# Optimization experiments

Hardware: AMD Instinct MI355X
Metric: run time of the kernel (lower is better)

The kernel has to match this reference:

```python
import jax, jax.numpy as jnp
import numpy as np


def _gcn(x, src, dst, W, b, n):
    # GCNConv: x' = D^{-1/2} (A + I) D^{-1/2} (x W) + b  (self-loops added)
    loop = jnp.arange(n, dtype=src.dtype)
    s = jnp.concatenate([src, loop])
    d = jnp.concatenate([dst, loop])
    deg = jax.ops.segment_sum(jnp.ones(s.shape[0], x.dtype), d, num_segments=n)
    dis = jnp.where(deg > 0, jax.lax.rsqrt(deg), jnp.zeros_like(deg))
    h = x @ W  # [n, out]
    msg = h[s] * (dis[s] * dis[d])[:, None]  # [E+n, out]
    return jax.ops.segment_sum(msg, d, num_segments=n) + b


def setup_inputs() -> dict:
    key = jax.random.key(0)
    ks = jax.random.split(key, 12)
    N0, N1, N2, N3, N4 = 100000, 200000, 400000, 800000, 1600000
    DEG = 6  # avg mesh degree

    def glorot(k, fi, fo):
        return jax.random.normal(k, (fi, fo), jnp.float32) * np.float32(np.sqrt(2.0 / (fi + fo)))

    def ei(k, n):
        return jax.random.randint(k, (2, DEG * n), 0, n, dtype=jnp.int32)

    return {
        "x": jax.random.normal(ks[0], (N0, 3), jnp.float32),
        "W1": glorot(ks[1], 3, 32), "b1": jnp.zeros((32,), jnp.float32),
        "W2": glorot(ks[2], 32, 64), "b2": jnp.zeros((64,), jnp.float32),
        "W3": glorot(ks[3], 64, 32), "b3": jnp.zeros((32,), jnp.float32),
        "W4": glorot(ks[4], 32, 3), "b4": jnp.zeros((3,), jnp.float32),
        "edge_index0": ei(ks[5], N0),
        "unpool1": jax.random.randint(ks[6], (N1,), 0, N0, dtype=jnp.int32),
        "edge_index1": ei(ks[7], N1),
        "unpool2": jax.random.randint(ks[8], (N2,), 0, N1, dtype=jnp.int32),
        "edge_index2": ei(ks[9], N2),
        "unpool3": jax.random.randint(ks[10], (N3,), 0, N2, dtype=jnp.int32),
        "edge_index3": ei(ks[11], N3),
        "unpool4": jax.random.randint(jax.random.fold_in(key, 99), (N4,), 0, N3, dtype=jnp.int32),
    }


def reference(x, W1, b1, W2, b2, W3, b3, W4, b4,
              edge_index0, unpool1, edge_index1, unpool2,
              edge_index2, unpool3, edge_index3, unpool4):
    N0 = x.shape[0]
    N1, N2, N3 = unpool1.shape[0], unpool2.shape[0], unpool3.shape[0]
    h = jax.nn.relu(_gcn(x, edge_index0[0], edge_index0[1], W1, b1, N0))
    h = h[unpool1]  # mesh_unpool stage 1: gather to finer mesh
    h = jax.nn.relu(_gcn(h, edge_index1[0], edge_index1[1], W2, b2, N1))
    h = h[unpool2]
    h = jax.nn.relu(_gcn(h, edge_index2[0], edge_index2[1], W3, b3, N2))
    h = h[unpool3]
    h = jax.nn.relu(_gcn(h, edge_index3[0], edge_index3[1], W4, b4, N3))
    return h[unpool4]  # final unpooled vertex features [N4, 3]
```

## Files before the change

kernel.cpp:

```cpp
#include <hip/hip_runtime.h>
#include <hip/hip_bf16.h>

typedef __hip_bfloat16 bf16;
typedef unsigned short u16;
typedef unsigned char u8;
typedef unsigned int u32;
typedef __attribute__((ext_vector_type(8))) unsigned short us8;

static __device__ __forceinline__ float b2f(bf16 v) { return __bfloat162float(v); }
static __device__ __forceinline__ float bfu2f(u32 u) {
    union { u32 i; float f; } c; c.i = u << 16; return c.f;
}
static __device__ __forceinline__ u16 f2bfu(float f) {
    u32 x = __float_as_uint(f);
    return (u16)((x + 0x7FFFu + ((x >> 16) & 1u)) >> 16);
}

#define TILE 4096
#define CBITS 12
#define CRANGE 4096
#define OUTB 26624
#define WF_W1 0
#define WF_B1 128
#define WF_W2 192
#define WF_B2 2240
#define WF_W3 2304
#define WF_W4 4352
#define WF_TOT 4608
#define RPT16(M) M(0) M(1) M(2) M(3) M(4) M(5) M(6) M(7) \
                 M(8) M(9) M(10) M(11) M(12) M(13) M(14) M(15)

struct SP {
    const int* src; const int* dst;
    int E, N, cap, nb, nblk, nbpad;
    int* gcur;
    u32* pairs;
    int* M;
    int* rowptr; float* dis; int* csr;
};
struct Pack {
    SP s[4];
    int poff[4];
    int boff[4];
};

__global__ void k_detect(const u16* __restrict__ xraw, int* __restrict__ flag) {
    __shared__ int s;
    if (threadIdx.x == 0) s = 0;
    __syncthreads();
    u16 u = xraw[threadIdx.x];
    int e = (u >> 7) & 0xFF;
    if (e >= 0x8F) atomicAdd(&s, 1);
    __syncthreads();
    if (threadIdx.x == 0) flag[0] = (s > 0) ? 1 : 0;
}

__global__ void k_prep_w(const void* W1, const void* b1, const void* W2,
                         const void* b2, const void* W3, const void* W4,
                         float* __restrict__ wf, const int* __restrict__ flag) {
    int t = blockIdx.x * 256 + threadIdx.x;
    int f32m = flag[0];
    const void* src; int off; int len;
    if      (t < WF_B1)  { src = W1; off = t - WF_W1; len = 96;  }
    else if (t < WF_W2)  { src = b1; off = t - WF_B1; len = 32;  }
    else if (t < WF_B2)  { src = W2; off = t - WF_W2; len = 2048;}
    else if (t < WF_W3)  { src = b2; off = t - WF_B2; len = 64;  }
    else if (t < WF_W4)  { src = W3; off = t - WF_W3; len = 2048;}
    else if (t < WF_TOT) { src = W4; off = t - WF_W4; len = 96;  }
    else return;
    if (off >= len) return;
    wf[t] = f32m ? ((const float*)src)[off] : b2f(((const bf16*)src)[off]);
}

__global__ void k_init(int* __restrict__ gcur_all, Pack pk) {
    int i = blockIdx.x * blockDim.x + threadIdx.x;
    if (i < 1024) gcur_all[i] = 0;
    if (i < 4) pk.s[i].rowptr[pk.s[i].N] = pk.s[i].E;
}

__global__ void __launch_bounds__(256) k_part_hist(Pack pk) {
    __shared__ int hist[256];
    int bid = blockIdx.x;
    int si = (bid >= pk.poff[3]) ? 3 : (bid >= pk.poff[2]) ? 2 : (bid >= pk.poff[1]) ? 1 : 0;
    const SP sp = pk.s[si];
    int lb = bid - pk.poff[si];
    int t = threadIdx.x;
    int n = min(TILE, sp.E - lb * TILE);
    const int* dstp = sp.dst + lb * TILE;

#define LOADK(k) int d##k; { int i = t + 256*(k); d##k = (i < n) ? dstp[i] : -1; }
    RPT16(LOADK)
#undef LOADK
    hist[t] = 0;
    __syncthreads();
#define HISTK(k) if (d##k >= 0) atomicAdd(&hist[d##k >> CBITS], 1);
    RPT16(HISTK)
#undef HISTK
    __syncthreads();
    int* Mrow = sp.M + (size_t)lb * sp.nbpad;
    for (int b = t; b < sp.nb; b += 256) Mrow[b] = hist[b];
}

__global__ void __launch_bounds__(256) k_part_scan(Pack pk) {
    __shared__ int buf[256];
    int bid = blockIdx.x;
    int si = (bid >= pk.boff[3]) ? 3 : (bid >= pk.boff[2]) ? 2 : (bid >= pk.boff[1]) ? 1 : 0;
    const SP sp = pk.s[si];
    int b = bid - pk.boff[si];
    int t = threadIdx.x;
    int nblk = sp.nblk, nbpad = sp.nbpad;
    int* M = sp.M;
    int carry = 0;
    for (int base = 0; base < nblk; base += 256) {
        int m = min(256, nblk - base);
        int v = (t < m) ? M[(size_t)(base + t) * nbpad + b] : 0;
        buf[t] = v;
        __syncthreads();
        for (int off = 1; off < 256; off <<= 1) {
            int w = (t >= off) ? buf[t - off] : 0;
            __syncthreads();
            buf[t] += w;
            __syncthreads();
        }
        int excl = buf[t] - v + carry;
        int ctot = buf[255];
        __syncthreads();
        if (t < m) M[(size_t)(base + t) * nbpad + b] = excl;
        carry += ctot;
    }
    if (t == 0) sp.gcur[b] = carry;
}

__global__ void __launch_bounds__(256) k_partition(Pack pk) {
    __shared__ u32 stage[TILE];
    __shared__ u8  bkt[TILE];
    __shared__ int hist[256];
    __shared__ int gofs[256];
    __shared__ int tmp[256];

    int bid = blockIdx.x;
    int si = (bid >= pk.poff[3]) ? 3 : (bid >= pk.poff[2]) ? 2 : (bid >= pk.poff[1]) ? 1 : 0;
    const SP sp = pk.s[si];
    int lb = bid - pk.poff[si];
    int t = threadIdx.x;
    int n = min(TILE, sp.E - lb * TILE);
    const int* dstp = sp.dst + lb * TILE;
    const int* srcp = sp.src + lb * TILE;

#define LOADK(k) int d##k, s##k; { int i = t + 256*(k); \
    if (i < n) { d##k = dstp[i]; s##k = srcp[i]; } else { d##k = -1; s##k = 0; } }
    RPT16(LOADK)
#undef LOADK

    hist[t] = 0;
    __syncthreads();
#define HISTK(k) if (d##k >= 0) atomicAdd(&hist[d##k >> CBITS], 1);
    RPT16(HISTK)
#undef HISTK
    __syncthreads();

    int h = hist[t];
    tmp[t] = h; __syncthreads();
    for (int off = 1; off < 256; off <<= 1) {
        int v = (t >= off) ? tmp[t - off] : 0;
        __syncthreads();
        tmp[t] += v;
        __syncthreads();
    }
    int lofs = tmp[t] - h;
    int gb = (t < sp.nb) ? sp.M[(size_t)lb * sp.nbpad + t] : 0;
    gofs[t] = gb - lofs;
    hist[t] = lofs;
    __syncthreads();

#define SCATK(k) if (d##k >= 0) { int b = d##k >> CBITS; \
    int pos = atomicAdd(&hist[b], 1); \
    stage[pos] = (((u32)d##k & 4095u) << 20) | (u32)s##k; \
    bkt[pos] = (u8)b; }
    RPT16(SCATK)
#undef SCATK
    __syncthreads();

    int cap = sp.cap;
    u32* pairs = sp.pairs;
    for (int i = t; i < n; i += 256) {
        int b = bkt[i];
        pairs[(size_t)b * cap + gofs[b] + i] = stage[i];
    }
}

__global__ void k_scan_bbase(Pack pk, int* __restrict__ bbase_all) {
    __shared__ int tmp[256];
    int si = blockIdx.x;
    int t = threadIdx.x;
    int nb = pk.s[si].nb;
    int v = (t < nb) ? pk.s[si].gcur[t] : 0;
    tmp[t] = v; __syncthreads();
    for (int off = 1; off < 256; off <<= 1) {
        int w = (t >= off) ? tmp[t - off] : 0;
        __syncthreads();
        tmp[t] += w;
        __syncthreads();
    }
    bbase_all[si * 256 + t] = tmp[t] - v;
}

__global__ void __launch_bounds__(512) k_build(Pack pk, const int* __restrict__ bbase_all) {
    __shared__ int hist[4096];
    __shared__ int outb[OUTB];
    __shared__ int tmp[512];

    int bid = blockIdx.x;
    int si = (bid >= pk.boff[3]) ? 3 : (bid >= pk.boff[2]) ? 2 : (bid >= pk.boff[1]) ? 1 : 0;
    const SP sp = pk.s[si];
    int b = bid - pk.boff[si];
    int t = threadIdx.x;

    int bbase = bbase_all[si * 256 + b];
    int tot = sp.gcur[b];
    const u32* p = sp.pairs + (size_t)b * sp.cap;
    const uint4* p4 = (const uint4*)p;
    int tot4 = tot >> 2;

    for (int i = t; i < 4096; i += 512) hist[i] = 0;
    __syncthreads();
    for (int i = t; i < tot4; i += 512) {
        uint4 u = p4[i];
        atomicAdd(&hist[u.x >> 20], 1);
        atomicAdd(&hist[u.y >> 20], 1);
        atomicAdd(&hist[u.z >> 20], 1);
        atomicAdd(&hist[u.w >> 20], 1);
    }
    for (int i = (tot4 << 2) + t; i < tot; i += 512)
        atomicAdd(&hist[p[i] >> 20], 1);
    __syncthreads();

    int lbase = t * 8;
    int cnt[8], cof[8];
    #pragma unroll
    for (int k = 0; k < 8; k++) cnt[k] = hist[lbase + k];
    int s = 0;
    #pragma unroll
    for (int k = 0; k < 8; k++) { cof[k] = s; s += cnt[k]; }
    tmp[t] = s; __syncthreads();
    for (int off = 1; off < 512; off <<= 1) {
        int v = (t >= off) ? tmp[t - off] : 0;
        __syncthreads();
        tmp[t] += v;
        __syncthreads();
    }
    int tb = tmp[t] - s;

    int nbase = b << CBITS;
    #pragma unroll
    for (int k = 0; k < 8; k++) {
        int bin = lbase + k;
        hist[bin] = tb + cof[k];
        int v = nbase + bin;
        if (v < sp.N) {
            sp.rowptr[v] = bbase + tb + cof[k];
            sp.dis[v] = rsqrtf((float)(cnt[k] + 1));
        }
    }
    __syncthreads();

    if (tot <= OUTB) {
        for (int i = t; i < tot4; i += 512) {
            uint4 u = p4[i];
            int pos;
            pos = atomicAdd(&hist[u.x >> 20], 1); outb[pos] = (int)(u.x & 0xFFFFFu);
            pos = atomicAdd(&hist[u.y >> 20], 1); outb[pos] = (int)(u.y & 0xFFFFFu);
            pos = atomicAdd(&hist[u.z >> 20], 1); outb[pos] = (int)(u.z & 0xFFFFFu);
            pos = atomicAdd(&hist[u.w >> 20], 1); outb[pos] = (int)(u.w & 0xFFFFFu);
        }
        for (int i = (tot4 << 2) + t; i < tot; i += 512) {
            u32 u = p[i];
            int pos = atomicAdd(&hist[u >> 20], 1);
            outb[pos] = (int)(u & 0xFFFFFu);
        }
        __syncthreads();
        for (int i = t; i < tot; i += 512)
            sp.csr[bbase + i] = outb[i];
    } else {
        for (int i = t; i < tot; i += 512) {
            u32 u = p[i];
            int pos = atomicAdd(&hist[u >> 20], 1);
            sp.csr[bbase + pos] = (int)(u & 0xFFFFFu);
        }
    }
}

template <int F, bool EXT>
__global__ void k_pre(const void* __restrict__ xin, const int* __restrict__ gidx,
                      const bf16* __restrict__ actin, const float* __restrict__ dis,
                      bf16* __restrict__ g, const int* __restrict__ flag, int total) {
    int i = blockIdx.x * blockDim.x + threadIdx.x;
    if (i >= total) return;
    int v = i / F;
    int f = i - v * F;
    float x;
    if (EXT) {
        if (flag[0]) x = ((const float*)xin)[i];
        else         x = b2f(((const bf16*)xin)[i]);
    } else {
        int row = gidx[v];
        x = b2f(actin[(size_t)row * F + f]);
    }
    g[i] = __float2bfloat16(dis[v] * x);
}

__global__ void __launch_bounds__(256, 1) k_fuse_mm_pre(
        const bf16* __restrict__ xt1, const int* __restrict__ up,
        const float* __restrict__ wf, const float* __restrict__ dis,
        bf16* __restrict__ g, int n) {
    const float* W = wf + WF_W1;
    const float* B = wf + WF_B1;
    int v = blockIdx.x * 256 + threadIdx.x;
    if (v >= n) return;
    int r = up[v];
    float x0 = b2f(xt1[(size_t)r * 3 + 0]);
    float x1 = b2f(xt1[(size_t)r * 3 + 1]);
    float x2 = b2f(xt1[(size_t)r * 3 + 2]);
    float dv = dis[v];
    #pragma unroll
    for (int f8 = 0; f8 < 4; f8++) {
        us8 ov;
        #pragma unroll
        for (int j = 0; j < 8; j++) {
            int f = f8 * 8 + j;
            float y = B[f];
            y = fmaf(x0, W[f], y);
            y = fmaf(x1, W[32 + f], y);
            y = fmaf(x2, W[64 + f], y);
            y = y > 0.f ? y : 0.f;
            ov[j] = f2bfu(dv * y);
        }
        *(us8*)(g + (size_t)v * 32 + f8 * 8) = ov;
    }
}

__global__ void __launch_bounds__(256, 1) k_fuse_mm2(
        const bf16* __restrict__ xt2, const float* __restrict__ wf,
        bf16* __restrict__ h, int n) {
    __shared__ float Xs[256 * 33];
    const float* W2f = wf + WF_W2;
    const float* B2f = wf + WF_B2;
    const float* W3f = wf + WF_W3;
    int v = blockIdx.x * 256 + threadIdx.x;
    if (v >= n) return;
    float* xs = &Xs[threadIdx.x * 33];
    #pragma unroll
    for (int k8 = 0; k8 < 4; k8++) {
        us8 xv = *(const us8*)(xt2 + (size_t)v * 32 + k8 * 8);
        #pragma unroll
        for (int j = 0; j < 8; j++) xs[k8 * 8 + j] = bfu2f((u32)(u16)xv[j]);
    }
    float acc[32];
    #pragma unroll
    for (int f = 0; f < 32; f++) acc[f] = 0.f;
    #pragma unroll
    for (int c = 0; c < 64; c += 32) {
        float y[32];
        #pragma unroll
        for (int f = 0; f < 32; f++) y[f] = B2f[c + f];
        #pragma unroll
        for (int k = 0; k < 32; k++) {
            float xk = xs[k];
            const float* wr = &W2f[k * 64 + c];
            #pragma unroll
            for (int f = 0; f < 32; f++) y[f] = fmaf(xk, wr[f], y[f]);
        }
        #pragma unroll
        for (int j = 0; j < 32; j++) {
            float yj = y[j] > 0.f ? y[j] : 0.f;
            const float* wr3 = &W3f[(c + j) * 32];
            #pragma unroll
            for (int f = 0; f < 32; f++) acc[f] = fmaf(yj, wr3[f], acc[f]);
        }
    }
    #pragma unroll
    for (int f8 = 0; f8 < 4; f8++) {
        us8 ov;
        #pragma unroll
        for (int j = 0; j < 8; j++) ov[j] = f2bfu(acc[f8 * 8 + j]);
        *(us8*)(h + (size_t)v * 32 + f8 * 8) = ov;
    }
}

template <int FIN, int FOUT>
__global__ void __launch_bounds__(256, 1) k_matmul_seq(
        const bf16* __restrict__ actin, const float* __restrict__ W,
        bf16* __restrict__ h, int n) {
    int v = blockIdx.x * blockDim.x + threadIdx.x;
    if (v >= n) return;
    float y[FOUT];
    #pragma unroll
    for (int f = 0; f < FOUT; f++) y[f] = 0.f;
    #pragma unroll
    for (int k8 = 0; k8 < FIN / 8; k8++) {
        us8 xv = *(const us8*)(actin + (size_t)v * FIN + k8 * 8);
        #pragma unroll
        for (int j = 0; j < 8; j++) {
            float xk = bfu2f((u32)(u16)xv[j]);
            const float* wrow = &W[(k8 * 8 + j) * FOUT];
            #pragma unroll
            for (int f = 0; f < FOUT; f++) y[f] = fmaf(xk, wrow[f], y[f]);
        }
    }
    if constexpr (FOUT % 8 == 0) {
        #pragma unroll
        for (int f8 = 0; f8 < FOUT / 8; f8++) {
            us8 ov;
            #pragma unroll
            for (int j = 0; j < 8; j++) ov[j] = f2bfu(y[f8 * 8 + j]);
            *(us8*)(h + (size_t)v * FOUT + f8 * 8) = ov;
        }
    } else {
        #pragma unroll
        for (int f = 0; f < FOUT; f++)
            h[(size_t)v * FOUT + f] = __float2bfloat16(y[f]);
    }
}

template <int FOUT, bool FINALIZE>
__global__ void __launch_bounds__(256) k_gather2v(
        const bf16* __restrict__ g, const int* __restrict__ rowptr,
        const int* __restrict__ csr, const float* __restrict__ dis,
        const void* __restrict__ bias, bf16* __restrict__ out,
        const int* __restrict__ flag, int totq, int E) {
    constexpr int Q = FOUT / 4;
    constexpr u32 W2 = FOUT / 2;
    int H = (totq + 1) >> 1;
    int i = blockIdx.x * blockDim.x + threadIdx.x;
    if (i >= H) return;
    int Em1 = E - 1;
    int e1 = i;
    int e2 = i + H;
    int e2c = (e2 < totq) ? e2 : e1;
    int v1 = e1 / Q, q1 = e1 - v1 * Q;
    int v2 = e2c / Q, q2 = e2c - v2 * Q;
    u32 qo1 = (u32)(q1 * 2), qo2 = (u32)(q2 * 2);
    const u32* g32 = (const u32*)g;

    uint2 sv1 = *(const uint2*)(g32 + (u32)v1 * W2 + qo1);
    uint2 sv2 = *(const uint2*)(g32 + (u32)v2 * W2 + qo2);
    float s10 = bfu2f(sv1.x & 0xFFFFu), s11 = bfu2f(sv1.x >> 16);
    float s12 = bfu2f(sv1.y & 0xFFFFu), s13 = bfu2f(sv1.y >> 16);
    float s20 = bfu2f(sv2.x & 0xFFFFu), s21 = bfu2f(sv2.x >> 16);
    float s22 = bfu2f(sv2.y & 0xFFFFu), s23 = bfu2f(sv2.y >> 16);

    int r1 = rowptr[v1]; int c1 = rowptr[v1 + 1] - r1;
    int r2 = rowptr[v2]; int c2 = rowptr[v2 + 1] - r2;
    int last1 = min(r1 + (c1 > 0 ? c1 - 1 : 0), Em1);
    int last2 = min(r2 + (c2 > 0 ? c2 - 1 : 0), Em1);
    int j1 = 0, j2 = 0;
    while (j1 < c1 || j2 < c2) {
        int i10 = min(r1 + j1 + 0, last1), i11 = min(r1 + j1 + 1, last1);
        int i12 = min(r1 + j1 + 2, last1), i13 = min(r1 + j1 + 3, last1);
        int i20 = min(r2 + j2 + 0, last2), i21 = min(r2 + j2 + 1, last2);
        int i22 = min(r2 + j2 + 2, last2), i23 = min(r2 + j2 + 3, last2);
        u32 u10 = (u32)csr[i10], u11 = (u32)csr[i11];
        u32 u12 = (u32)csr[i12], u13 = (u32)csr[i13];
        u32 u20 = (u32)csr[i20], u21 = (u32)csr[i21];
        u32 u22 = (u32)csr[i22], u23 = (u32)csr[i23];
        uint2 a10 = *(const uint2*)(g32 + u10 * W2 + qo1);
        uint2 a11 = *(const uint2*)(g32 + u11 * W2 + qo1);
        uint2 a12 = *(const uint2*)(g32 + u12 * W2 + qo1);
        uint2 a13 = *(const uint2*)(g32 + u13 * W2 + qo1);
        uint2 a20 = *(const uint2*)(g32 + u20 * W2 + qo2);
        uint2 a21 = *(const uint2*)(g32 + u21 * W2 + qo2);
        uint2 a22 = *(const uint2*)(g32 + u22 * W2 + qo2);
        uint2 a23 = *(const uint2*)(g32 + u23 * W2 + qo2);
        if (j1 + 0 >= c1) { a10.x = 0; a10.y = 0; }
        if (j1 + 1 >= c1) { a11.x = 0; a11.y = 0; }
        if (j1 + 2 >= c1) { a12.x = 0; a12.y = 0; }
        if (j1 + 3 >= c1) { a13.x = 0; a13.y = 0; }
        if (j2 + 0 >= c2) { a20.x = 0; a20.y = 0; }
        if (j2 + 1 >= c2) { a21.x = 0; a21.y = 0; }
        if (j2 + 2 >= c2) { a22.x = 0; a22.y = 0; }
        if (j2 + 3 >= c2) { a23.x = 0; a23.y = 0; }
        s10 += bfu2f(a10.x & 0xFFFFu) + bfu2f(a11.x & 0xFFFFu)
             + bfu2f(a12.x & 0xFFFFu) + bfu2f(a13.x & 0xFFFFu);
        s11 += bfu2f(a10.x >> 16) + bfu2f(a11.x >> 16)
             + bfu2f(a12.x >> 16) + bfu2f(a13.x >> 16);
        s12 += bfu2f(a10.y & 0xFFFFu) + bfu2f(a11.y & 0xFFFFu)
             + bfu2f(a12.y & 0xFFFFu) + bfu2f(a13.y & 0xFFFFu);
        s13 += bfu2f(a10.y >> 16) + bfu2f(a11.y >> 16)
             + bfu2f(a12.y >> 16) + bfu2f(a13.y >> 16);
        s20 += bfu2f(a20.x & 0xFFFFu) + bfu2f(a21.x & 0xFFFFu)
             + bfu2f(a22.x & 0xFFFFu) + bfu2f(a23.x & 0xFFFFu);
        s21 += bfu2f(a20.x >> 16) + bfu2f(a21.x >> 16)
             + bfu2f(a22.x >> 16) + bfu2f(a23.x >> 16);
        s22 += bfu2f(a20.y & 0xFFFFu) + bfu2f(a21.y & 0xFFFFu)
             + bfu2f(a22.y & 0xFFFFu) + bfu2f(a23.y & 0xFFFFu);
        s23 += bfu2f(a20.y >> 16) + bfu2f(a21.y >> 16)
             + bfu2f(a22.y >> 16) + bfu2f(a23.y >> 16);
        j1 += 4; j2 += 4;
    }
    float dv1 = dis[v1], dv2 = dis[v2];
    float o1[4] = {s10, s11, s12, s13};
    float o2[4] = {s20, s21, s22, s23};
    uint2 w1, w2;
    if (FINALIZE) {
        int f32m = flag[0];
        #pragma unroll
        for (int k = 0; k < 4; k++) {
            int f1 = q1 * 4 + k, f2 = q2 * 4 + k;
            float bf1 = f32m ? ((const float*)bias)[f1] : b2f(((const bf16*)bias)[f1]);
            float bf2 = f32m ? ((const float*)bias)[f2] : b2f(((const bf16*)bias)[f2]);
            o1[k] = fmaf(dv1, o1[k], bf1); o1[k] = o1[k] > 0.f ? o1[k] : 0.f;
            o2[k] = fmaf(dv2, o2[k], bf2); o2[k] = o2[k] > 0.f ? o2[k] : 0.f;
        }
    } else {
        #pragma unroll
        for (int k = 0; k < 4; k++) { o1[k] *= dv1; o2[k] *= dv2; }
    }
    w1.x = (u32)f2bfu(o1[0]) | ((u32)f2bfu(o1[1]) << 16);
    w1.y = (u32)f2bfu(o1[2]) | ((u32)f2bfu(o1[3]) << 16);
    w2.x = (u32)f2bfu(o2[0]) | ((u32)f2bfu(o2[1]) << 16);
    w2.y = (u32)f2bfu(o2[2]) | ((u32)f2bfu(o2[3]) << 16);
    u32* o32 = (u32*)out;
    *(uint2*)(o32 + (u32)v1 * W2 + qo1) = w1;
    if (e2 < totq) *(uint2*)(o32 + (u32)v2 * W2 + qo2) = w2;
}

template <int FOUT, bool FINALIZE>
__global__ void __launch_bounds__(256) k_gather2(
        const bf16* __restrict__ g, const int* __restrict__ rowptr,
        const int* __restrict__ csr, const float* __restrict__ dis,
        const void* __restrict__ bias, bf16* __restrict__ out,
        const int* __restrict__ flag, int total, int E) {
    int H = (total + 1) >> 1;
    int i = blockIdx.x * blockDim.x + threadIdx.x;
    if (i >= H) return;
    int Em1 = E - 1;
    int e1 = i;
    int e2 = i + H;
    int e2c = (e2 < total) ? e2 : e1;
    int v1 = e1 / FOUT, f1 = e1 - v1 * FOUT;
    int v2 = e2c / FOUT, f2 = e2c - v2 * FOUT;
    float s1 = b2f(g[e1]);
    float s2 = b2f(g[e2c]);
    int r1 = rowptr[v1]; int c1 = rowptr[v1 + 1] - r1;
    int r2 = rowptr[v2]; int c2 = rowptr[v2 + 1] - r2;
    int last1 = min(r1 + (c1 > 0 ? c1 - 1 : 0), Em1);
    int last2 = min(r2 + (c2 > 0 ? c2 - 1 : 0), Em1);
    int j1 = 0, j2 = 0;
    while (j1 < c1 || j2 < c2) {
        int i10 = min(r1 + j1 + 0, last1), i11 = min(r1 + j1 + 1, last1);
        int i12 = min(r1 + j1 + 2, last1), i13 = min(r1 + j1 + 3, last1);
        int i20 = min(r2 + j2 + 0, last2), i21 = min(r2 + j2 + 1, last2);
        int i22 = min(r2 + j2 + 2, last2), i23 = min(r2 + j2 + 3, last2);
        int u10 = csr[i10], u11 = csr[i11], u12 = csr[i12], u13 = csr[i13];
        int u20 = csr[i20], u21 = csr[i21], u22 = csr[i22], u23 = csr[i23];
        float a10 = b2f(g[(size_t)u10 * FOUT + f1]);
        float a11 = b2f(g[(size_t)u11 * FOUT + f1]);
        float a12 = b2f(g[(size_t)u12 * FOUT + f1]);
        float a13 = b2f(g[(size_t)u13 * FOUT + f1]);
        float a20 = b2f(g[(size_t)u20 * FOUT + f2]);
        float a21 = b2f(g[(size_t)u21 * FOUT + f2]);
        float a22 = b2f(g[(size_t)u22 * FOUT + f2]);
        float a23 = b2f(g[(size_t)u23 * FOUT + f2]);
        s1 += ((j1 + 0 < c1 ? a10 : 0.f) + (j1 + 1 < c1 ? a11 : 0.f))
            + ((j1 + 2 < c1 ? a12 : 0.f) + (j1 + 3 < c1 ? a13 : 0.f));
        s2 += ((j2 + 0 < c2 ? a20 : 0.f) + (j2 + 1 < c2 ? a21 : 0.f))
            + ((j2 + 2 < c2 ? a22 : 0.f) + (j2 + 3 < c2 ? a23 : 0.f));
        j1 += 4; j2 += 4;
    }
    float dv1 = dis[v1], dv2 = dis[v2];
    float o1, o2;
    if (FINALIZE) {
        float bf1 = flag[0] ? ((const float*)bias)[f1] : b2f(((const bf16*)bias)[f1]);
        float bf2 = flag[0] ? ((const float*)bias)[f2] : b2f(((const bf16*)bias)[f2]);
        o1 = fmaf(dv1, s1, bf1); o1 = o1 > 0.f ? o1 : 0.f;
        o2 = fmaf(dv2, s2, bf2); o2 = o2 > 0.f ? o2 : 0.f;
    } else {
        o1 = dv1 * s1;
        o2 = dv2 * s2;
    }
    out[e1] = __float2bfloat16(o1);
    if (e2 < total) out[e2] = __float2bfloat16(o2);
}

__global__ void k_gather_out(const bf16* __restrict__ act, const int* __restrict__ idx,
                             void* __restrict__ out, const int* __restrict__ flag, int n) {
    int u = blockIdx.x * blockDim.x + threadIdx.x;
    if (u >= n) return;
    size_t r = (size_t)idx[u];
    float v0 = b2f(act[3 * r + 0]);
    float v1 = b2f(act[3 * r + 1]);
    float v2 = b2f(act[3 * r + 2]);
    if (flag[0]) {
        float* o = (float*)out;
        o[3 * (size_t)u + 0] = v0; o[3 * (size_t)u + 1] = v1; o[3 * (size_t)u + 2] = v2;
    } else {
        bf16* o = (bf16*)out;
        o[3 * (size_t)u + 0] = __float2bfloat16(v0);
        o[3 * (size_t)u + 1] = __float2bfloat16(v1);
        o[3 * (size_t)u + 2] = __float2bfloat16(v2);
    }
}

static inline int cdiv(long long a, long long b) { return (int)((a + b - 1) / b); }

extern "C" void kernel_launch(void* const* d_in, const int* in_sizes, int n_in,
                              void* d_out, int out_size, void* d_ws, size_t ws_size,
                              hipStream_t stream) {
    const void* x  = d_in[0];
    const void* W1 = d_in[1]; const void* b1 = d_in[2];
    const void* W2 = d_in[3]; const void* b2 = d_in[4];
    const void* W3 = d_in[5]; const void* b3 = d_in[6];
    const void* W4 = d_in[7]; const void* b4 = d_in[8];
    const int* e0  = (const int*)d_in[9];
    const int* up1 = (const int*)d_in[10];
    const int* e1  = (const int*)d_in[11];
    const int* up2 = (const int*)d_in[12];
    const int* e2  = (const int*)d_in[13];
    const int* up3 = (const int*)d_in[14];
    const int* e3  = (const int*)d_in[15];
    const int* up4 = (const int*)d_in[16];

    const int N0 = in_sizes[0] / 3;
    const int N1 = in_sizes[10];
    const int N2 = in_sizes[12];
    const int N3 = in_sizes[14];
    const int N4 = in_sizes[16];
    const int E0 = in_sizes[9] / 2, E1 = in_sizes[11] / 2;
    const int E2 = in_sizes[13] / 2, E3 = in_sizes[15] / 2;

    int Ns[4] = {N0, N1, N2, N3};
    int Es[4] = {E0, E1, E2, E3};
    const int* srcs[4] = {e0, e1, e2, e3};
    const int* dsts[4] = {e0 + E0, e1 + E1, e2 + E2, e3 + E3};

    size_t gmax = (size_t)N0 * 3;
    if ((size_t)N1 * 32 > gmax) gmax = (size_t)N1 * 32;
    if ((size_t)N2 * 32 > gmax) gmax = (size_t)N2 * 32;
    if ((size_t)N3 * 3  > gmax) gmax = (size_t)N3 * 3;
    size_t amax = (size_t)N0 * 32;
    if ((size_t)N1 * 64 > amax) amax = (size_t)N1 * 64;
    if ((size_t)N2 * 32 > amax) amax = (size_t)N2 * 32;
    if ((size_t)N3 * 3  > amax) amax = (size_t)N3 * 3;
    gmax = (gmax + 7) & ~(size_t)7;
    amax = (amax + 7) & ~(size_t)7;

    Pack pk;
    char* p = (char*)d_ws;
    int* flag = (int*)p;            p += 256;
    float* wf = (float*)p;          p += WF_TOT * 4;
    int* gcur_all = (int*)p;        p += 1024 * 4;
    int* bbase_all = (int*)p;       p += 1024 * 4;

    for (int s = 0; s < 4; s++) {
        pk.s[s].src = srcs[s]; pk.s[s].dst = dsts[s];
        pk.s[s].E = Es[s]; pk.s[s].N = Ns[s];
        int nb = cdiv(Ns[s], CRANGE);
        pk.s[s].nb = nb;
        pk.s[s].nblk = cdiv(Es[s], TILE);
        pk.s[s].nbpad = (nb + 15) & ~15;
        pk.s[s].cap = (Es[s] / nb + Es[s] / (8 * nb) + 256 + 3) & ~3;
        pk.s[s].gcur = gcur_all + s * 256;
        pk.s[s].M = (int*)p;        p += (size_t)pk.s[s].nblk * pk.s[s].nbpad * 4;
        pk.s[s].rowptr = (int*)p;   p += ((size_t)(Ns[s] + 1 + 3) & ~(size_t)3) * 4;
        pk.s[s].dis = (float*)p;    p += ((size_t)(Ns[s] + 3) & ~(size_t)3) * 4;
    }
    for (int s = 0; s < 4; s++) {
        pk.s[s].csr = (int*)p;      p += ((size_t)(Es[s] + 3) & ~(size_t)3) * 4;
    }

    char* U = (char*)(((size_t)p + 15) & ~(size_t)15);
    size_t pairsBytes = 0;
    for (int s = 0; s < 4; s++) {
        pk.s[s].pairs = (u32*)(U + pairsBytes);
        pairsBytes += (size_t)pk.s[s].cap * pk.s[s].nb * 4;
    }
    bf16* g   = (bf16*)U;
    bf16* act = g + gmax;
    bf16* xt  = act + amax;

    int ptot = 0, btot = 0;
    for (int s = 0; s < 4; s++) {
        pk.poff[s] = ptot; ptot += pk.s[s].nblk;
        pk.boff[s] = btot; btot += pk.s[s].nb;
    }

    const int B = 256;

    k_detect<<<1, 256, 0, stream>>>((const u16*)x, flag);
    k_prep_w<<<cdiv(WF_TOT, B), B, 0, stream>>>(W1, b1, W2, b2, W3, W4, wf, flag);
    k_init<<<4, 256, 0, stream>>>(gcur_all, pk);
    k_part_hist<<<ptot, B, 0, stream>>>(pk);
    k_part_scan<<<btot, B, 0, stream>>>(pk);
    k_partition<<<ptot, B, 0, stream>>>(pk);
    k_scan_bbase<<<4, B, 0, stream>>>(pk, bbase_all);
    k_build<<<btot, 512, 0, stream>>>(pk, bbase_all);

    {
        int T = N0 * 3, Hh = (T + 1) >> 1;
        k_pre<3, true><<<cdiv(T, B), B, 0, stream>>>(
            x, nullptr, nullptr, pk.s[0].dis, g, flag, T);
        k_gather2<3, false><<<cdiv(Hh, B), B, 0, stream>>>(
            g, pk.s[0].rowptr, pk.s[0].csr, pk.s[0].dis, nullptr, xt, flag, T, E0);
    }

    k_fuse_mm_pre<<<cdiv(N1, B), B, 0, stream>>>(
        xt, up1, wf, pk.s[1].dis, g, N1);

    {
        int Tq = N1 * 8, Hq = (Tq + 1) >> 1;
        k_gather2v<32, false><<<cdiv(Hq, B), B, 0, stream>>>(
            g, pk.s[1].rowptr, pk.s[1].csr, pk.s[1].dis, nullptr, xt, flag, Tq, E1);
    }

    k_fuse_mm2<<<cdiv(N1, B), B, 0, stream>>>(xt, wf, act, N1);

    {
        int Tq = N2 * 8, Hq = (Tq + 1) >> 1;
        k_pre<32, false><<<cdiv((long long)N2 * 32, B), B, 0, stream>>>(
            nullptr, up2, act, pk.s[2].dis, g, flag, N2 * 32);
        k_gather2v<32, true><<<cdiv(Hq, B), B, 0, stream>>>(
            g, pk.s[2].rowptr, pk.s[2].csr, pk.s[2].dis, b3, act, flag, Tq, E2);
    }

    {
        int T = N3 * 3, Hh = (T + 1) >> 1;
        k_matmul_seq<32, 3><<<cdiv(N2, B), B, 0, stream>>>(act, wf + WF_W4, xt, N2);
        k_pre<3, false><<<cdiv(T, B), B, 0, stream>>>(
            nullptr, up3, xt, pk.s[3].dis, g, flag, T);
        k_gather2<3, true><<<cdiv(Hh, B), B, 0, stream>>>(
            g, pk.s[3].rowptr, pk.s[3].csr, pk.s[3].dis, b4, act, flag, T, E3);
    }

    k_gather_out<<<cdiv(N4, B), B, 0, stream>>>(act, up4, d_out, flag, N4);
}
```

Measured before the change: 465.0 us.

## Compute fused W2/W3 matmul with bf16 MFMA instead of scalar FMAs

Rewrites the fused 32->64->32 layer-2/layer-3 matmul to use 16x16x32 bf16 MFMA instructions, with each wavefront handling 16 rows. The weight-prep kernel now also builds pre-swizzled bf16 MFMA B-fragments of W2 and W3. The intermediate ReLU activations are rounded to bf16 and staged through shared memory, which adds a precision loss compared with the fp32 scalar path. The goal is to replace about 4K scalar FMAs per row, which ran at one block per CU with heavy register use.

```diff
diff --git a/kernel.cpp b/kernel.cpp
--- a/kernel.cpp
+++ b/kernel.cpp
@@ -6,6 +6,8 @@
 typedef unsigned char u8;
 typedef unsigned int u32;
 typedef __attribute__((ext_vector_type(8))) unsigned short us8;
+typedef __attribute__((ext_vector_type(8))) short short8;
+typedef __attribute__((ext_vector_type(4))) float f32x4;
 
 static __device__ __forceinline__ float b2f(bf16 v) { return __bfloat162float(v); }
 static __device__ __forceinline__ float bfu2f(u32 u) {
@@ -27,6 +29,7 @@
 #define WF_W3 2304
 #define WF_W4 4352
 #define WF_TOT 4608
+#define NFRAG 4096
 #define RPT16(M) M(0) M(1) M(2) M(3) M(4) M(5) M(6) M(7) \
                  M(8) M(9) M(10) M(11) M(12) M(13) M(14) M(15)
 
@@ -57,19 +60,39 @@
 
 __global__ void k_prep_w(const void* W1, const void* b1, const void* W2,
                          const void* b2, const void* W3, const void* W4,
-                         float* __restrict__ wf, const int* __restrict__ flag) {
+                         float* __restrict__ wf, u16* __restrict__ wfrag,
+                         const int* __restrict__ flag) {
     int t = blockIdx.x * 256 + threadIdx.x;
     int f32m = flag[0];
-    const void* src; int off; int len;
-    if      (t < WF_B1)  { src = W1; off = t - WF_W1; len = 96;  }
-    else if (t < WF_W2)  { src = b1; off = t - WF_B1; len = 32;  }
-    else if (t < WF_B2)  { src = W2; off = t - WF_W2; len = 2048;}
-    else if (t < WF_W3)  { src = b2; off = t - WF_B2; len = 64;  }
-    else if (t < WF_W4)  { src = W3; off = t - WF_W3; len = 2048;}
-    else if (t < WF_TOT) { src = W4; off = t - WF_W4; len = 96;  }
-    else return;
-    if (off >= len) return;
-    wf[t] = f32m ? ((const float*)src)[off] : b2f(((const bf16*)src)[off]);
+    if (t < WF_TOT) {
+        const void* src; int off; int len;
+        if      (t < WF_B1)  { src = W1; off = t - WF_W1; len = 96;  }
+        else if (t < WF_W2)  { src = b1; off = t - WF_B1; len = 32;  }
+        else if (t < WF_B2)  { src = W2; off = t - WF_W2; len = 2048;}
+        else if (t < WF_W3)  { src = b2; off = t - WF_B2; len = 64;  }
+        else if (t < WF_W4)  { src = W3; off = t - WF_W3; len = 2048;}
+        else                 { src = W4; off = t - WF_W4; len = 96;  }
+        if (off >= len) return;
+        wf[t] = f32m ? ((const float*)src)[off] : b2f(((const bf16*)src)[off]);
+    } else if (t < WF_TOT + NFRAG) {
+        int idx = t - WF_TOT;
+        int sec = idx >> 9;
+        int l = (idx >> 3) & 63;
+        int i = idx & 7;
+        int cl = l & 15, grp = l >> 4;
+        float val;
+        if (sec < 4) {
+            int k = grp * 8 + i, col = sec * 16 + cl;
+            val = f32m ? ((const float*)W2)[k * 64 + col]
+                       : b2f(((const bf16*)W2)[k * 64 + col]);
+        } else {
+            int q = sec - 4, kt = q >> 1, t2 = q & 1;
+            int k = kt * 32 + grp * 8 + i, col = t2 * 16 + cl;
+            val = f32m ? ((const float*)W3)[k * 32 + col]
+                       : b2f(((const bf16*)W3)[k * 32 + col]);
+        }
+        wfrag[idx] = f2bfu(val);
+    }
 }
 
 __global__ void k_init(int* __restrict__ gcur_all, Pack pk) {
@@ -339,52 +362,49 @@
     }
 }
 
-__global__ void __launch_bounds__(256, 1) k_fuse_mm2(
-        const bf16* __restrict__ xt2, const float* __restrict__ wf,
-        bf16* __restrict__ h, int n) {
-    __shared__ float Xs[256 * 33];
-    const float* W2f = wf + WF_W2;
+__global__ void __launch_bounds__(256) k_fuse_mm2(
+        const bf16* __restrict__ xt2, const u16* __restrict__ wfrag,
+        const float* __restrict__ wf, bf16* __restrict__ h, int n) {
+    __shared__ u16 Ys[4][16 * 72];
+    __shared__ u16 Hs[4][16 * 32];
     const float* B2f = wf + WF_B2;
-    const float* W3f = wf + WF_W3;
-    int v = blockIdx.x * 256 + threadIdx.x;
-    if (v >= n) return;
-    float* xs = &Xs[threadIdx.x * 33];
+    int t = threadIdx.x;
+    int w = t >> 6, l = t & 63;
+    int cl = l & 15, grp = l >> 4;
+    int v0 = blockIdx.x * 64 + w * 16;
+    if (v0 >= n) return;
+    int ar = v0 + cl; ar = ar < n ? ar : n - 1;
+    short8 a1 = *(const short8*)(xt2 + (size_t)ar * 32 + grp * 8);
+    const short8* wf2 = (const short8*)wfrag;
+    const short8* wf3 = (const short8*)(wfrag + 2048);
+    u16* Y = Ys[w];
+    u16* H = Hs[w];
     #pragma unroll
-    for (int k8 = 0; k8 < 4; k8++) {
-        us8 xv = *(const us8*)(xt2 + (size_t)v * 32 + k8 * 8);
+    for (int t4 = 0; t4 < 4; t4++) {
+        f32x4 acc = {0.f, 0.f, 0.f, 0.f};
+        acc = __builtin_amdgcn_mfma_f32_16x16x32_bf16(a1, wf2[t4 * 64 + l], acc, 0, 0, 0);
+        float bias = B2f[t4 * 16 + cl];
         #pragma unroll
-        for (int j = 0; j < 8; j++) xs[k8 * 8 + j] = bfu2f((u32)(u16)xv[j]);
-    }
-    float acc[32];
+        for (int r = 0; r < 4; r++) {
+            float y = acc[r] + bias;
+            y = y > 0.f ? y : 0.f;
+            Y[(4 * grp + r) * 72 + t4 * 16 + cl] = f2bfu(y);
+        }
+    }
+    short8 a20 = *(const short8*)(Y + cl * 72 + grp * 8);
+    short8 a21 = *(const short8*)(Y + cl * 72 + 32 + grp * 8);
     #pragma unroll
-    for (int f = 0; f < 32; f++) acc[f] = 0.f;
-    #pragma unroll
-    for (int c = 0; c < 64; c += 32) {
-        float y[32];
+    for (int t2 = 0; t2 < 2; t2++) {
+        f32x4 acc = {0.f, 0.f, 0.f, 0.f};
+        acc = __builtin_amdgcn_mfma_f32_16x16x32_bf16(a20, wf3[t2 * 64 + l], acc, 0, 0, 0);
+        acc = __builtin_amdgcn_mfma_f32_16x16x32_bf16(a21, wf3[(2 + t2) * 64 + l], acc, 0, 0, 0);
         #pragma unroll
-        for (int f = 0; f < 32; f++) y[f] = B2f[c + f];
-        #pragma unroll
-        for (int k = 0; k < 32; k++) {
-            float xk = xs[k];
-            const float* wr = &W2f[k * 64 + c];
-            #pragma unroll
-            for (int f = 0; f < 32; f++) y[f] = fmaf(xk, wr[f], y[f]);
-        }
-        #pragma unroll
-        for (int j = 0; j < 32; j++) {
-            float yj = y[j] > 0.f ? y[j] : 0.f;
-            const float* wr3 = &W3f[(c + j) * 32];
-            #pragma unroll
-            for (int f = 0; f < 32; f++) acc[f] = fmaf(yj, wr3[f], acc[f]);
-        }
-    }
-    #pragma unroll
-    for (int f8 = 0; f8 < 4; f8++) {
-        us8 ov;
-        #pragma unroll
-        for (int j = 0; j < 8; j++) ov[j] = f2bfu(acc[f8 * 8 + j]);
-        *(us8*)(h + (size_t)v * 32 + f8 * 8) = ov;
-    }
+        for (int r = 0; r < 4; r++)
+            H[(4 * grp + r) * 32 + t2 * 16 + cl] = f2bfu(acc[r]);
+    }
+    int orow = v0 + (l >> 2);
+    if (orow < n)
+        *(us8*)(h + (size_t)orow * 32 + (l & 3) * 8) = *(const us8*)(H + l * 8);
 }
 
 template <int FIN, int FOUT>
@@ -648,6 +668,7 @@
     char* p = (char*)d_ws;
     int* flag = (int*)p;            p += 256;
     float* wf = (float*)p;          p += WF_TOT * 4;
+    u16* wfrag = (u16*)p;           p += NFRAG * 2;
     int* gcur_all = (int*)p;        p += 1024 * 4;
     int* bbase_all = (int*)p;       p += 1024 * 4;
 
@@ -687,7 +708,8 @@
     const int B = 256;
 
     k_detect<<<1, 256, 0, stream>>>((const u16*)x, flag);
-    k_prep_w<<<cdiv(WF_TOT, B), B, 0, stream>>>(W1, b1, W2, b2, W3, W4, wf, flag);
+    k_prep_w<<<cdiv(WF_TOT + NFRAG, B), B, 0, stream>>>(
+        W1, b1, W2, b2, W3, W4, wf, wfrag, flag);
     k_init<<<4, 256, 0, stream>>>(gcur_all, pk);
     k_part_hist<<<ptot, B, 0, stream>>>(pk);
     k_part_scan<<<btot, B, 0, stream>>>(pk);
@@ -712,7 +734,7 @@
             g, pk.s[1].rowptr, pk.s[1].csr, pk.s[1].dis, nullptr, xt, flag, Tq, E1);
     }
 
-    k_fuse_mm2<<<cdiv(N1, B), B, 0, stream>>>(xt, wf, act, N1);
+    k_fuse_mm2<<<cdiv(N1, 64), B, 0, stream>>>(xt, wfrag, wf, act, N1);
 
     {
         int Tq = N2 * 8, Hq = (Tq + 1) >> 1;
```

Result: faster. 438.4 us (-5.7%).
